# Performance work log

Hardware: AMD Instinct MI355X
Metric: run time of the kernel (lower is better)

The kernel has to match this reference:

```python
import jax, jax.numpy as jnp
import numpy as np

# dims
P = 49      # per-participant input dim
G = 8       # group-only (dyadic/triadic) dim
R = 26      # robot input dim
PH = 20     # participant GRU hidden dim
GF = 16     # group_fc output dim
H = 64      # main RNN hidden dim
T = 512     # seq_len
B = 2048    # batch
D = 2 * P + G + R  # 132 total feature dim, layout [p1|p2|group|robot]


def _gru_cell(x, h, Wih, Whh, bih, bhh):
    # torch.nn.GRUCell math: gates ordered (r, z, n)
    gi = x @ Wih.T + bih          # (B, 3*hid)
    gh = h @ Whh.T + bhh          # (B, 3*hid)
    ir, iz, inn = jnp.split(gi, 3, axis=-1)
    hr, hz, hn = jnp.split(gh, 3, axis=-1)
    r = jax.nn.sigmoid(ir + hr)
    z = jax.nn.sigmoid(iz + hz)
    n = jnp.tanh(inn + r * hn)
    return (1.0 - z) * n + z * h


def setup_inputs() -> dict:
    key = jax.random.key(0)
    ks = jax.random.split(key, 16)

    def u(k, shape, fan):
        b = 1.0 / np.sqrt(fan)
        return jax.random.uniform(k, shape, jnp.float32, -b, b)

    rnn_in = GF + R  # 42: group_fc output concat robot slice
    return {
        "sequence": jax.random.normal(ks[0], (T, B, D), jnp.float32),
        # p1 GRUCell
        "p1_Wih": u(ks[1], (3 * PH, P), PH),
        "p1_Whh": u(ks[2], (3 * PH, PH), PH),
        "p1_bih": u(ks[3], (3 * PH,), PH),
        "p1_bhh": u(ks[4], (3 * PH,), PH),
        # p2 GRUCell
        "p2_Wih": u(ks[5], (3 * PH, P), PH),
        "p2_Whh": u(ks[6], (3 * PH, PH), PH),
        "p2_bih": u(ks[7], (3 * PH,), PH),
        "p2_bhh": u(ks[8], (3 * PH,), PH),
        # group_fc: Linear(2*PH+G -> GF) + ReLU
        "g_W": u(ks[9], (GF, 2 * PH + G), 2 * PH + G),
        "g_b": u(ks[10], (GF,), 2 * PH + G),
        # main GRUCell
        "r_Wih": u(ks[11], (3 * H, rnn_in), H),
        "r_Whh": u(ks[12], (3 * H, H), H),
        "r_bih": u(ks[13], (3 * H,), H),
        "r_bhh": u(ks[14], (3 * H,), H),
    }


def reference(sequence, p1_Wih, p1_Whh, p1_bih, p1_bhh,
              p2_Wih, p2_Whh, p2_bih, p2_bhh,
              g_W, g_b, r_Wih, r_Whh, r_bih, r_bhh):
    batch = sequence.shape[1]

    def step(carry, xt):
        h1, h2, h = carry
        # data_helper slices: [p1 | p2 | group | robot]
        x_p1 = xt[:, :P]
        x_p2 = xt[:, P:2 * P]
        x_g = xt[:, 2 * P:2 * P + G]
        x_r = xt[:, 2 * P + G:]
        h1 = _gru_cell(x_p1, h1, p1_Wih, p1_Whh, p1_bih, p1_bhh)
        h2 = _gru_cell(x_p2, h2, p2_Wih, p2_Whh, p2_bih, p2_bhh)
        g = jax.nn.relu(jnp.concatenate([h1, h2, x_g], axis=1) @ g_W.T + g_b)
        inp = jnp.concatenate([g, x_r], axis=1)  # (B, GF+R)
        h = _gru_cell(inp, h, r_Wih, r_Whh, r_bih, r_bhh)
        return (h1, h2, h), h

    init = (jnp.zeros((batch, PH), jnp.float32),
            jnp.zeros((batch, PH), jnp.float32),
            jnp.zeros((batch, H), jnp.float32))
    _, all_hidden = jax.lax.scan(step, init, sequence)  # (T, B, H)
    return all_hidden
```

## Files before the change

kernel.cpp:

```cpp
#include <hip/hip_runtime.h>


#define T_STEPS 512
#define B_BATCH 2048
#define D_IN    132
#define NROWS   8
#define NBLOCKS 256
#define STEP2   (B_BATCH * D_IN / 2)
#define NITEMS  (NROWS * 66)

typedef _Float16 f16x8 __attribute__((ext_vector_type(8)));
typedef float    f32x4 __attribute__((ext_vector_type(4)));
typedef float    f32x2 __attribute__((ext_vector_type(2)));

#define MFMA16(a, b, c) __builtin_amdgcn_mfma_f32_16x16x32_f16((a), (b), (c), 0, 0, 0)

#define PX    1024
#define AP1   0
#define AP2   2048
#define AG    4096
#define AR    8192
#define AP1H  12288
#define AP2H  14336
#define AH    16384
#define LDS_N 18432

#define BARRIER() do { \
    asm volatile("s_waitcnt lgkmcnt(0)\n\ts_barrier" ::: "memory"); \
    __builtin_amdgcn_sched_barrier(0); \
  } while (0)

__device__ __forceinline__ int swz(int row, int col) {
  return row * 64 + (((col >> 3) ^ (row & 7)) << 3) + (col & 7);
}

__device__ __forceinline__ f16x8 ldsFrag(const _Float16* lds, int base, int lane, int kt) {
  int row = lane & 7;
  int blk = ((kt << 2) + (lane >> 4)) ^ row;
  return *reinterpret_cast<const f16x8*>(lds + base + row * 64 + blk * 8);
}

__device__ __forceinline__ f16x8 mkfrag(const float* W, int row, int K, int kbase, int lane, bool ok) {
  f16x8 f;
  int k0 = kbase + ((lane >> 4) << 3);
#pragma unroll
  for (int j = 0; j < 8; ++j) {
    int k = k0 + j;
    float v = 0.0f;
    if (ok && k < K) v = W[row * K + k];
    f[j] = (_Float16)v;
  }
  return f;
}

__device__ __forceinline__ float rcpf(float x) { return __builtin_amdgcn_rcpf(x); }
__device__ __forceinline__ float ex2(float x)  { return __builtin_amdgcn_exp2f(x); }

__global__ __launch_bounds__(512, 2) void rnn_fused(
    const float* __restrict__ seq,
    const float* __restrict__ p1Wih, const float* __restrict__ p1Whh,
    const float* __restrict__ p1bih, const float* __restrict__ p1bhh,
    const float* __restrict__ p2Wih, const float* __restrict__ p2Whh,
    const float* __restrict__ p2bih, const float* __restrict__ p2bhh,
    const float* __restrict__ gW,    const float* __restrict__ gb,
    const float* __restrict__ rWih,  const float* __restrict__ rWhh,
    const float* __restrict__ rbih,  const float* __restrict__ rbhh,
    float* __restrict__ out)
{
  __shared__ __align__(16) _Float16 lds[LDS_N];
  const int tid  = threadIdx.x;
  const int lane = tid & 63;
  const int wv   = tid >> 6;
  const bool isR = (wv < 4);
  const int b0   = blockIdx.x * NROWS;
  const int ul   = lane & 15;
  const bool lo  = (lane < 32);
  const int grp4 = ((lane >> 4) & 1) * 4;
  const int row0 = grp4 + (lo ? 0 : 2);
  const float C1 = 1.44269504089f;

  for (int i = tid; i < LDS_N; i += 512) lds[i] = (_Float16)0.0f;

  f16x8 fghr[2], fghz[2], fghn[2], fgir[2], fgiz[2], fgin[2];
  float nbr2 = 0, nbz2 = 0, bin2 = 0, bhn2 = 0;
  float hq2[2] = {0, 0};
  int stAddr[3][2]; int ldIdx[3] = {0, 0, 0};
  bool stOK[3] = {false, false, false}, isP[3] = {false, false, false};
  int ahw2[2] = {0, 0};
  float* outp = nullptr;

  f16x8 pgi0[2], pgi1[2], pgi2[2], pgh0, pgh1, pgh2, fgw[2];
  float nbr = 0, nbz = 0, bin = 0, bhn = 0, gbias = 0;
  float h1q2[2] = {0, 0};
  int apB = 0, aphB = 0, up = 0; bool uok = false;
  int agw2[2] = {0, 0}, aphw2[2] = {0, 0}, arw2[2] = {0, 0};

  if (isR) {
    const int uR = wv * 16 + ul;
    fghr[0] = mkfrag(rWhh,       uR, 64,  0, lane, true);
    fghr[1] = mkfrag(rWhh,       uR, 64, 32, lane, true);
    fghz[0] = mkfrag(rWhh,  64 + uR, 64,  0, lane, true);
    fghz[1] = mkfrag(rWhh,  64 + uR, 64, 32, lane, true);
    fghn[0] = mkfrag(rWhh, 128 + uR, 64,  0, lane, true);
    fghn[1] = mkfrag(rWhh, 128 + uR, 64, 32, lane, true);
    fgir[0] = mkfrag(rWih,       uR, 42,  0, lane, true);
    fgir[1] = mkfrag(rWih,       uR, 42, 32, lane, true);
    fgiz[0] = mkfrag(rWih,  64 + uR, 42,  0, lane, true);
    fgiz[1] = mkfrag(rWih,  64 + uR, 42, 32, lane, true);
    fgin[0] = mkfrag(rWih, 128 + uR, 42,  0, lane, true);
    fgin[1] = mkfrag(rWih, 128 + uR, 42, 32, lane, true);
    nbr2 = -C1 * (rbih[uR] + rbhh[uR]);
    nbz2 = -C1 * (rbih[64 + uR] + rbhh[64 + uR]);
    bin2 = rbih[128 + uR]; bhn2 = rbhh[128 + uR];
    ahw2[0] = AH + swz(row0, uR);
    ahw2[1] = AH + swz(row0 + 1, uR);
#pragma unroll
    for (int it = 0; it < 3; ++it) {
      int ii = it * 256 + (wv * 64 + lane);
      stOK[it] = (ii < NITEMS);
      int iic = stOK[it] ? ii : (NITEMS - 1);
      ldIdx[it] = iic;
      int rr = iic / 66, c2 = iic % 66;
      isP[it] = (c2 < 49);
#pragma unroll
      for (int e = 0; e < 2; ++e) {
        int c = c2 * 2 + e;
        int tb, col;
        if (c < 49)       { tb = AP1; col = c; }
        else if (c < 98)  { tb = AP2; col = c - 49; }
        else if (c < 106) { tb = AG;  col = 40 + (c - 98); }
        else              { tb = AR;  col = 16 + (c - 106); }
        stAddr[it][e] = tb + swz(rr, col);
      }
    }
    outp = out + (size_t)(b0 + row0) * 64 + uR;
  } else {
    const int pw  = wv - 4;
    const int gru = pw >> 1;
    const int s   = pw & 1;
    const float* Wih = gru ? p2Wih : p1Wih;
    const float* Whh = gru ? p2Whh : p1Whh;
    const float* bih = gru ? p2bih : p1bih;
    const float* bhh = gru ? p2bhh : p1bhh;
    up  = s * 16 + ul;
    uok = (up < 20);
    pgi0[0] = mkfrag(Wih,      up, 49,  0, lane, uok);
    pgi0[1] = mkfrag(Wih,      up, 49, 32, lane, uok);
    pgh0    = mkfrag(Whh,      up, 20,  0, lane, uok);
    pgi1[0] = mkfrag(Wih, 20 + up, 49,  0, lane, uok);
    pgi1[1] = mkfrag(Wih, 20 + up, 49, 32, lane, uok);
    pgh1    = mkfrag(Whh, 20 + up, 20,  0, lane, uok);
    pgi2[0] = mkfrag(Wih, 40 + up, 49,  0, lane, uok);
    pgi2[1] = mkfrag(Wih, 40 + up, 49, 32, lane, uok);
    pgh2    = mkfrag(Whh, 40 + up, 20,  0, lane, uok);
    fgw[0]  = mkfrag(gW, ul, 48,  0, lane, true);
    fgw[1]  = mkfrag(gW, ul, 48, 32, lane, true);
    gbias = gb[ul];
    if (uok) {
      nbr = -C1 * (bih[up] + bhh[up]);
      nbz = -C1 * (bih[20 + up] + bhh[20 + up]);
      bin = bih[40 + up]; bhn = bhh[40 + up];
    }
    apB  = gru ? AP2  : AP1;
    aphB = gru ? AP2H : AP1H;
    const int gcol = gru ? (20 + up) : up;
#pragma unroll
    for (int j = 0; j < 2; ++j) {
      agw2[j]  = AG + swz(row0 + j, gcol);
      aphw2[j] = aphB + swz(row0 + j, up);
      arw2[j]  = AR + swz(row0 + j, ul);
    }
  }

  __syncthreads();

  f32x2 rs0[3], rs1[3], rs2[3], rs3[3];
  const f32x2* spR = nullptr;
  if (isR) {
    const f32x2* sp = reinterpret_cast<const f32x2*>(seq) + (size_t)b0 * (D_IN / 2);
#pragma unroll
    for (int it = 0; it < 3; ++it) {
      rs0[it] = sp[ldIdx[it]];
      rs1[it] = sp[(size_t)1 * STEP2 + ldIdx[it]];
      rs2[it] = sp[(size_t)2 * STEP2 + ldIdx[it]];
      rs3[it] = sp[(size_t)3 * STEP2 + ldIdx[it]];
    }
#pragma unroll
    for (int it = 0; it < 3; ++it) if (stOK[it]) {
      lds[stAddr[it][0]] = (_Float16)rs0[it][0];
      lds[stAddr[it][1]] = (_Float16)rs0[it][1];
    }
    spR = sp + (size_t)4 * STEP2;
  }
  __syncthreads();

  const f32x4 Z = {0.0f, 0.0f, 0.0f, 0.0f};

  auto rPhase = [&](int offP, int offGR, int slotA, int ahR, int ahW,
                    bool doMain, bool doStage, f32x2 (&rsStage)[3], f32x2 (&rsLoad)[3],
                    bool advance) {
#pragma unroll
    for (int it = 0; it < 3; ++it) rsLoad[it] = spR[ldIdx[it]];
    if (advance) spR += STEP2;
    if (doStage) {
#pragma unroll
      for (int it = 0; it < 3; ++it) if (stOK[it]) {
        const int off = isP[it] ? offP : offGR;
        lds[off + stAddr[it][0]] = (_Float16)rsStage[it][0];
        lds[off + stAddr[it][1]] = (_Float16)rsStage[it][1];
      }
    }
    if (doMain) {
      f16x8 r0  = ldsFrag(lds, AR + slotA, lane, 0);
      f16x8 r1  = ldsFrag(lds, AR + slotA, lane, 1);
      f16x8 h0  = ldsFrag(lds, AH + ahR, lane, 0);
      f16x8 h1f = ldsFrag(lds, AH + ahR, lane, 1);
      f32x4 cR  = MFMA16(h0, fghr[0], Z);
      f32x4 cZ  = MFMA16(h0, fghz[0], Z);
      f32x4 cHN = MFMA16(h0, fghn[0], Z);
      cR  = MFMA16(h1f, fghr[1], cR);
      cZ  = MFMA16(h1f, fghz[1], cZ);
      cHN = MFMA16(h1f, fghn[1], cHN);
      cR  = MFMA16(r0, fgir[0], cR);  cR  = MFMA16(r1, fgir[1], cR);
      cZ  = MFMA16(r0, fgiz[0], cZ);  cZ  = MFMA16(r1, fgiz[1], cZ);
      f32x4 cIN = MFMA16(r0, fgin[0], Z);
      cIN = MFMA16(r1, fgin[1], cIN);
      float xRv[2] = { lo ? cR[0]  : cR[2],  lo ? cR[1]  : cR[3]  };
      float xZv[2] = { lo ? cZ[0]  : cZ[2],  lo ? cZ[1]  : cZ[3]  };
      float xHv[2] = { lo ? cHN[0] : cHN[2], lo ? cHN[1] : cHN[3] };
      float xIv[2] = { lo ? cIN[0] : cIN[2], lo ? cIN[1] : cIN[3] };
#pragma unroll
      for (int j = 0; j < 2; ++j) {
        float r   = rcpf(1.0f + ex2(fmaf(xRv[j], -C1, nbr2)));
        float z   = rcpf(1.0f + ex2(fmaf(xZv[j], -C1, nbz2)));
        float pre = fmaf(r, xHv[j] + bhn2, xIv[j] + bin2);
        float e2  = ex2(pre * (2.0f * C1));
        float n   = 1.0f - 2.0f * rcpf(1.0f + e2);
        float hv  = fmaf(z, hq2[j] - n, n);
        hq2[j] = hv;
        outp[j * 64] = hv;
        lds[ahW + ahw2[j]] = (_Float16)hv;
      }
      outp += (size_t)B_BATCH * 64;
    }
  };

  auto pPhase = [&](int pj, int agWr, int aphWr, int gSlot, bool doComp, bool doGate) {
    if (doComp) {
      f16x8 a0 = ldsFrag(lds, apB + pj, lane, 0);
      f16x8 a1 = ldsFrag(lds, apB + pj, lane, 1);
      f16x8 ah = ldsFrag(lds, aphB + pj, lane, 0);
      f32x4 aR  = MFMA16(a0, pgi0[0], Z);
      f32x4 aZ  = MFMA16(a0, pgi1[0], Z);
      f32x4 aIN = MFMA16(a0, pgi2[0], Z);
      f32x4 aHN = MFMA16(ah, pgh2, Z);
      aR  = MFMA16(a1, pgi0[1], aR);  aR = MFMA16(ah, pgh0, aR);
      aZ  = MFMA16(a1, pgi1[1], aZ);  aZ = MFMA16(ah, pgh1, aZ);
      aIN = MFMA16(a1, pgi2[1], aIN);
      float xRv[2] = { lo ? aR[0]  : aR[2],  lo ? aR[1]  : aR[3]  };
      float xZv[2] = { lo ? aZ[0]  : aZ[2],  lo ? aZ[1]  : aZ[3]  };
      float xIv[2] = { lo ? aIN[0] : aIN[2], lo ? aIN[1] : aIN[3] };
      float xHv[2] = { lo ? aHN[0] : aHN[2], lo ? aHN[1] : aHN[3] };
#pragma unroll
      for (int j = 0; j < 2; ++j) {
        float r   = rcpf(1.0f + ex2(fmaf(xRv[j], -C1, nbr)));
        float z   = rcpf(1.0f + ex2(fmaf(xZv[j], -C1, nbz)));
        float pre = fmaf(r, xHv[j] + bhn, xIv[j] + bin);
        float e2  = ex2(pre * (2.0f * C1));
        float n   = 1.0f - 2.0f * rcpf(1.0f + e2);
        float hv  = fmaf(z, h1q2[j] - n, n);
        h1q2[j] = hv;
        if (uok) {
          _Float16 hh = (_Float16)hv;
          lds[agWr + agw2[j]]  = hh;
          lds[aphWr + aphw2[j]] = hh;
        }
      }
    }
    if (doGate) {
      f16x8 g0 = ldsFrag(lds, AG + gSlot, lane, 0);
      f16x8 g1 = ldsFrag(lds, AG + gSlot, lane, 1);
      f32x4 cG = MFMA16(g0, fgw[0], Z);
      cG = MFMA16(g1, fgw[1], cG);
      float gv0 = lo ? cG[0] : cG[2], gv1 = lo ? cG[1] : cG[3];
      lds[gSlot + arw2[0]] = (_Float16)fmaxf(gv0 + gbias, 0.0f);
      lds[gSlot + arw2[1]] = (_Float16)fmaxf(gv1 + gbias, 0.0f);
    }
  };

  for (int i = 0; i < T_STEPS / 4; ++i) {
    const bool i0 = (i == 0);
    const int f0 = 4 * i;
    if (isR) rPhase(PX, PX, 2 * PX, PX, 0, !i0, true, rs1, rs0, (f0 + 5 < T_STEPS));
    else     pPhase(0, 0, PX, 3 * PX, true, !i0);
    BARRIER();
    if (isR) rPhase(0, 2 * PX, 3 * PX, 0, PX, !i0, true, rs2, rs1, (f0 + 6 < T_STEPS));
    else     pPhase(PX, PX, 0, 0, true, true);
    BARRIER();
    if (isR) rPhase(PX, 3 * PX, 0, PX, 0, true, true, rs3, rs2, (f0 + 7 < T_STEPS));
    else     pPhase(0, 2 * PX, PX, PX, true, true);
    BARRIER();
    if (isR) rPhase(0, 0, PX, 0, PX, true, (i != T_STEPS / 4 - 1), rs0, rs3,
                    (f0 + 8 < T_STEPS));
    else     pPhase(PX, 3 * PX, 0, 2 * PX, true, true);
    BARRIER();
  }
  if (isR) rPhase(0, 0, 2 * PX, PX, 0, true, false, rs0, rs1, false);
  else     pPhase(0, 0, PX, 3 * PX, false, true);
  BARRIER();
  if (isR) rPhase(0, 0, 3 * PX, 0, PX, true, false, rs0, rs1, false);
}

extern "C" void kernel_launch(void* const* d_in, const int* in_sizes, int n_in,
                              void* d_out, int out_size, void* d_ws, size_t ws_size,
                              hipStream_t stream) {
  (void)in_sizes; (void)n_in; (void)d_ws; (void)ws_size; (void)out_size;
  const float* seq   = (const float*)d_in[0];
  const float* p1Wih = (const float*)d_in[1];
  const float* p1Whh = (const float*)d_in[2];
  const float* p1bih = (const float*)d_in[3];
  const float* p1bhh = (const float*)d_in[4];
  const float* p2Wih = (const float*)d_in[5];
  const float* p2Whh = (const float*)d_in[6];
  const float* p2bih = (const float*)d_in[7];
  const float* p2bhh = (const float*)d_in[8];
  const float* gW    = (const float*)d_in[9];
  const float* gb    = (const float*)d_in[10];
  const float* rWih  = (const float*)d_in[11];
  const float* rWhh  = (const float*)d_in[12];
  const float* rbih  = (const float*)d_in[13];
  const float* rbhh  = (const float*)d_in[14];
  float* out = (float*)d_out;
  hipLaunchKernelGGL(rnn_fused, dim3(NBLOCKS), dim3(512), 0, stream,
                     seq, p1Wih, p1Whh, p1bih, p1bhh,
                     p2Wih, p2Whh, p2bih, p2bhh,
                     gW, gb, rWih, rWhh, rbih, rbhh, out);
}
```

Measured before the change: 304.7 us.

## Load participant inputs directly into registers as MFMA fragments, bypassing LDS staging

The participant GRU waves now read their own 49-wide input slices from global memory straight into registers, laid out as MFMA A-fragments, and prefetch two steps ahead. The R waves now stage only the group and robot columns through LDS. This removes the p1/p2 LDS staging buffers and the associated LDS stores and loads, shrinking LDS use and the R waves' per-step load work. In exchange, each participant wave issues uncoalesced 16-byte global loads every step and holds extra registers for the prefetched inputs. The fragment rows also read past column 49 into neighbouring features, which relies on the matching weight columns being zero-padded.

```diff
diff --git a/kernel.cpp b/kernel.cpp
--- a/kernel.cpp
+++ b/kernel.cpp
@@ -7,7 +7,8 @@
 #define NROWS   8
 #define NBLOCKS 256
 #define STEP2   (B_BATCH * D_IN / 2)
-#define NITEMS  (NROWS * 66)
+#define STEPF   (B_BATCH * D_IN)
+#define NGR     (NROWS * 17)
 
 typedef _Float16 f16x8 __attribute__((ext_vector_type(8)));
 typedef float    f32x4 __attribute__((ext_vector_type(4)));
@@ -16,14 +17,12 @@
 #define MFMA16(a, b, c) __builtin_amdgcn_mfma_f32_16x16x32_f16((a), (b), (c), 0, 0, 0)
 
 #define PX    1024
-#define AP1   0
-#define AP2   2048
-#define AG    4096
-#define AR    8192
-#define AP1H  12288
-#define AP2H  14336
-#define AH    16384
-#define LDS_N 18432
+#define AG    0
+#define AR    4096
+#define AP1H  8192
+#define AP2H  10240
+#define AH    12288
+#define LDS_N 14336
 
 #define BARRIER() do { \
     asm volatile("s_waitcnt lgkmcnt(0)\n\ts_barrier" ::: "memory"); \
@@ -84,15 +83,14 @@
   f16x8 fghr[2], fghz[2], fghn[2], fgir[2], fgiz[2], fgin[2];
   float nbr2 = 0, nbz2 = 0, bin2 = 0, bhn2 = 0;
   float hq2[2] = {0, 0};
-  int stAddr[3][2]; int ldIdx[3] = {0, 0, 0};
-  bool stOK[3] = {false, false, false}, isP[3] = {false, false, false};
+  int stA0 = 0, stA1 = 0, ldIdx = 0; bool stOK = false;
   int ahw2[2] = {0, 0};
   float* outp = nullptr;
 
   f16x8 pgi0[2], pgi1[2], pgi2[2], pgh0, pgh1, pgh2, fgw[2];
   float nbr = 0, nbz = 0, bin = 0, bhn = 0, gbias = 0;
   float h1q2[2] = {0, 0};
-  int apB = 0, aphB = 0, up = 0; bool uok = false;
+  int aphB = 0, up = 0; bool uok = false;
   int agw2[2] = {0, 0}, aphw2[2] = {0, 0}, arw2[2] = {0, 0};
 
   if (isR) {
@@ -114,24 +112,22 @@
     bin2 = rbih[128 + uR]; bhn2 = rbhh[128 + uR];
     ahw2[0] = AH + swz(row0, uR);
     ahw2[1] = AH + swz(row0 + 1, uR);
-#pragma unroll
-    for (int it = 0; it < 3; ++it) {
-      int ii = it * 256 + (wv * 64 + lane);
-      stOK[it] = (ii < NITEMS);
-      int iic = stOK[it] ? ii : (NITEMS - 1);
-      ldIdx[it] = iic;
-      int rr = iic / 66, c2 = iic % 66;
-      isP[it] = (c2 < 49);
+    {
+      int ii = wv * 64 + lane;
+      stOK = (ii < NGR);
+      int iic = stOK ? ii : (NGR - 1);
+      int rr = iic / 17, c2 = 49 + iic % 17;
+      ldIdx = rr * 66 + c2;
+      int a[2];
 #pragma unroll
       for (int e = 0; e < 2; ++e) {
         int c = c2 * 2 + e;
         int tb, col;
-        if (c < 49)       { tb = AP1; col = c; }
-        else if (c < 98)  { tb = AP2; col = c - 49; }
-        else if (c < 106) { tb = AG;  col = 40 + (c - 98); }
-        else              { tb = AR;  col = 16 + (c - 106); }
-        stAddr[it][e] = tb + swz(rr, col);
+        if (c < 106) { tb = AG; col = 40 + (c - 98); }
+        else         { tb = AR; col = 16 + (c - 106); }
+        a[e] = tb + swz(rr, col);
       }
+      stA0 = a[0]; stA1 = a[1];
     }
     outp = out + (size_t)(b0 + row0) * 64 + uR;
   } else {
@@ -161,7 +157,6 @@
       nbz = -C1 * (bih[20 + up] + bhh[20 + up]);
       bin = bih[40 + up]; bhn = bhh[40 + up];
     }
-    apB  = gru ? AP2  : AP1;
     aphB = gru ? AP2H : AP1H;
     const int gcol = gru ? (20 + up) : up;
 #pragma unroll
@@ -174,41 +169,46 @@
 
   __syncthreads();
 
-  f32x2 rs0[3], rs1[3], rs2[3], rs3[3];
+  f32x2 rs0{}, rs1{}, rs2{}, rs3{};
   const f32x2* spR = nullptr;
+  f32x4 xsA[4], xsB[4];
+  const float* xp = nullptr;
   if (isR) {
     const f32x2* sp = reinterpret_cast<const f32x2*>(seq) + (size_t)b0 * (D_IN / 2);
-#pragma unroll
-    for (int it = 0; it < 3; ++it) {
-      rs0[it] = sp[ldIdx[it]];
-      rs1[it] = sp[(size_t)1 * STEP2 + ldIdx[it]];
-      rs2[it] = sp[(size_t)2 * STEP2 + ldIdx[it]];
-      rs3[it] = sp[(size_t)3 * STEP2 + ldIdx[it]];
-    }
-#pragma unroll
-    for (int it = 0; it < 3; ++it) if (stOK[it]) {
-      lds[stAddr[it][0]] = (_Float16)rs0[it][0];
-      lds[stAddr[it][1]] = (_Float16)rs0[it][1];
+    rs0 = sp[ldIdx];
+    rs1 = sp[(size_t)1 * STEP2 + ldIdx];
+    rs2 = sp[(size_t)2 * STEP2 + ldIdx];
+    rs3 = sp[(size_t)3 * STEP2 + ldIdx];
+    if (stOK) {
+      lds[stA0] = (_Float16)rs0[0];
+      lds[stA1] = (_Float16)rs0[1];
     }
     spR = sp + (size_t)4 * STEP2;
+  } else {
+    const int gru = (wv - 4) >> 1;
+    const float* xb = seq + ((size_t)(b0 + (lane & 7)) * D_IN + gru * 49 + ((lane >> 4) << 3));
+    xsA[0] = *reinterpret_cast<const f32x4*>(xb + 0);
+    xsA[1] = *reinterpret_cast<const f32x4*>(xb + 4);
+    xsA[2] = *reinterpret_cast<const f32x4*>(xb + 32);
+    xsA[3] = *reinterpret_cast<const f32x4*>(xb + 36);
+    xsB[0] = *reinterpret_cast<const f32x4*>(xb + STEPF + 0);
+    xsB[1] = *reinterpret_cast<const f32x4*>(xb + STEPF + 4);
+    xsB[2] = *reinterpret_cast<const f32x4*>(xb + STEPF + 32);
+    xsB[3] = *reinterpret_cast<const f32x4*>(xb + STEPF + 36);
+    xp = xb + (size_t)2 * STEPF;
   }
   __syncthreads();
 
   const f32x4 Z = {0.0f, 0.0f, 0.0f, 0.0f};
 
-  auto rPhase = [&](int offP, int offGR, int slotA, int ahR, int ahW,
-                    bool doMain, bool doStage, f32x2 (&rsStage)[3], f32x2 (&rsLoad)[3],
+  auto rPhase = [&](int offGR, int slotA, int ahR, int ahW,
+                    bool doMain, bool doStage, f32x2& rsStage, f32x2& rsLoad,
                     bool advance) {
-#pragma unroll
-    for (int it = 0; it < 3; ++it) rsLoad[it] = spR[ldIdx[it]];
+    rsLoad = spR[ldIdx];
     if (advance) spR += STEP2;
-    if (doStage) {
-#pragma unroll
-      for (int it = 0; it < 3; ++it) if (stOK[it]) {
-        const int off = isP[it] ? offP : offGR;
-        lds[off + stAddr[it][0]] = (_Float16)rsStage[it][0];
-        lds[off + stAddr[it][1]] = (_Float16)rsStage[it][1];
-      }
+    if (doStage && stOK) {
+      lds[offGR + stA0] = (_Float16)rsStage[0];
+      lds[offGR + stA1] = (_Float16)rsStage[1];
     }
     if (doMain) {
       f16x8 r0  = ldsFrag(lds, AR + slotA, lane, 0);
@@ -245,10 +245,22 @@
     }
   };
 
-  auto pPhase = [&](int pj, int agWr, int aphWr, int gSlot, bool doComp, bool doGate) {
+  auto pPhase = [&](int pj, int agWr, int aphWr, int gSlot, bool doComp, bool doGate,
+                    f32x4 (&xs)[4], bool advX) {
     if (doComp) {
-      f16x8 a0 = ldsFrag(lds, apB + pj, lane, 0);
-      f16x8 a1 = ldsFrag(lds, apB + pj, lane, 1);
+      f16x8 a0, a1;
+#pragma unroll
+      for (int j = 0; j < 4; ++j) {
+        a0[j]     = (_Float16)xs[0][j];
+        a0[4 + j] = (_Float16)xs[1][j];
+        a1[j]     = (_Float16)xs[2][j];
+        a1[4 + j] = (_Float16)xs[3][j];
+      }
+      xs[0] = *reinterpret_cast<const f32x4*>(xp + 0);
+      xs[1] = *reinterpret_cast<const f32x4*>(xp + 4);
+      xs[2] = *reinterpret_cast<const f32x4*>(xp + 32);
+      xs[3] = *reinterpret_cast<const f32x4*>(xp + 36);
+      if (advX) xp += STEPF;
       f16x8 ah = ldsFrag(lds, aphB + pj, lane, 0);
       f32x4 aR  = MFMA16(a0, pgi0[0], Z);
       f32x4 aZ  = MFMA16(a0, pgi1[0], Z);
@@ -291,24 +303,24 @@
   for (int i = 0; i < T_STEPS / 4; ++i) {
     const bool i0 = (i == 0);
     const int f0 = 4 * i;
-    if (isR) rPhase(PX, PX, 2 * PX, PX, 0, !i0, true, rs1, rs0, (f0 + 5 < T_STEPS));
-    else     pPhase(0, 0, PX, 3 * PX, true, !i0);
+    if (isR) rPhase(PX, 2 * PX, PX, 0, !i0, true, rs1, rs0, (f0 + 5 < T_STEPS));
+    else     pPhase(0, 0, PX, 3 * PX, true, !i0, xsA, (f0 + 3 < T_STEPS));
     BARRIER();
-    if (isR) rPhase(0, 2 * PX, 3 * PX, 0, PX, !i0, true, rs2, rs1, (f0 + 6 < T_STEPS));
-    else     pPhase(PX, PX, 0, 0, true, true);
+    if (isR) rPhase(2 * PX, 3 * PX, 0, PX, !i0, true, rs2, rs1, (f0 + 6 < T_STEPS));
+    else     pPhase(PX, PX, 0, 0, true, true, xsB, (f0 + 4 < T_STEPS));
     BARRIER();
-    if (isR) rPhase(PX, 3 * PX, 0, PX, 0, true, true, rs3, rs2, (f0 + 7 < T_STEPS));
-    else     pPhase(0, 2 * PX, PX, PX, true, true);
+    if (isR) rPhase(3 * PX, 0, PX, 0, true, true, rs3, rs2, (f0 + 7 < T_STEPS));
+    else     pPhase(0, 2 * PX, PX, PX, true, true, xsA, (f0 + 5 < T_STEPS));
     BARRIER();
-    if (isR) rPhase(0, 0, PX, 0, PX, true, (i != T_STEPS / 4 - 1), rs0, rs3,
+    if (isR) rPhase(0, PX, 0, PX, true, (i != T_STEPS / 4 - 1), rs0, rs3,
                     (f0 + 8 < T_STEPS));
-    else     pPhase(PX, 3 * PX, 0, 2 * PX, true, true);
+    else     pPhase(PX, 3 * PX, 0, 2 * PX, true, true, xsB, (f0 + 6 < T_STEPS));
     BARRIER();
   }
-  if (isR) rPhase(0, 0, 2 * PX, PX, 0, true, false, rs0, rs1, false);
-  else     pPhase(0, 0, PX, 3 * PX, false, true);
+  if (isR) rPhase(0, 2 * PX, PX, 0, true, false, rs0, rs1, false);
+  else     pPhase(0, 0, PX, 3 * PX, false, true, xsA, false);
   BARRIER();
-  if (isR) rPhase(0, 0, 3 * PX, 0, PX, true, false, rs0, rs1, false);
+  if (isR) rPhase(0, 3 * PX, 0, PX, true, false, rs0, rs1, false);
 }
 
 extern "C" void kernel_launch(void* const* d_in, const int* in_sizes, int n_in,
```

Result: slower. 352.3 us (+15.6%).
